# Kernel optimization log

Measured on AMD Instinct MI355X. Metric: run time of the kernel, lower is better.

The kernel has to match this reference:

```python
import jax, jax.numpy as jnp
import numpy as np

B, S, D, H = 2, 2048, 1024, 16
HD = D // H


def setup_inputs() -> dict:
    key = jax.random.key(0)
    ks = jax.random.split(key, 9)
    s = 1.0 / np.sqrt(D)
    return {
        "qx": jax.random.normal(ks[0], (B, S, D), jnp.float32),
        "kx": jax.random.normal(ks[1], (B, S, D), jnp.float32),
        "vx": jax.random.normal(ks[2], (B, S, D), jnp.float32),
        "mask": jnp.tril(jnp.ones((S, S), jnp.int32))[None, None],  # [1,1,S,S] causal
        "Wq": jax.random.uniform(ks[3], (D, D), jnp.float32, -s, s),
        "bq": jax.random.uniform(ks[4], (D,), jnp.float32, -s, s),
        "Wk": jax.random.uniform(ks[5], (D, D), jnp.float32, -s, s),
        "bk": jax.random.uniform(ks[6], (D,), jnp.float32, -s, s),
        "Wv": jax.random.uniform(ks[7], (D, D), jnp.float32, -s, s),
        "bv": jax.random.uniform(ks[8], (D,), jnp.float32, -s, s),
    }


def reference(qx, kx, vx, mask, Wq, bq, Wk, bk, Wv, bv):
    bat, seq_len, d_model = qx.shape
    # torch Linear: y = x @ W.T + b
    q = qx @ Wq.T + bq
    k = kx @ Wk.T + bk
    v = vx @ Wv.T + bv
    # [b, h, s, hd]
    q = q.reshape(bat, seq_len, H, HD).transpose(0, 2, 1, 3)
    k = k.reshape(bat, seq_len, H, HD).transpose(0, 2, 1, 3)
    v = v.reshape(bat, seq_len, H, HD).transpose(0, 2, 1, 3)
    # NOTE: original scales by sqrt(d_model), not sqrt(head_dim)
    attn_weight = jnp.einsum('bhqd,bhkd->bhqk', q, k) / jnp.sqrt(
        jnp.asarray(d_model, q.dtype))
    attn_weight = jnp.where(mask == 0, -jnp.inf, attn_weight)
    attn_score = jax.nn.softmax(attn_weight, axis=-1)
    attn_output = jnp.einsum('bhqk,bhkd->bhqd', attn_score, v)
    return attn_output.transpose(0, 2, 1, 3).reshape(bat, seq_len, d_model)
```

## Files before the change

kernel.cpp:

```cpp
#include <hip/hip_runtime.h>


typedef __attribute__((ext_vector_type(8))) short short8;
typedef __attribute__((ext_vector_type(4))) short shortx4;
typedef __attribute__((ext_vector_type(4))) float floatx4;

#define NEGBIG (-1.0e30f)
#define QSCALE 0.04508422002778011f

__device__ __forceinline__ float bf2f(ushort u) {
    union { unsigned int i; float f; } x; x.i = ((unsigned int)u) << 16; return x.f;
}
__device__ __forceinline__ ushort f2bf(float f) {
    union { unsigned int i; float f; } x; x.f = f;
    return (ushort)((x.i + 0x7FFFu + ((x.i >> 16) & 1u)) >> 16);
}
__device__ __forceinline__ void gl_lds16(const void* g, void* l) {
    __builtin_amdgcn_global_load_lds(
        (const __attribute__((address_space(1))) unsigned int*)g,
        (__attribute__((address_space(3))) unsigned int*)l, 16, 0, 0);
}

__global__ void detect_dtype(const unsigned int* __restrict__ w, int* __restrict__ flag) {
    const int lane = threadIdx.x;
    int hits = 0;
    for (int i = 0; i < 16; ++i) {
        unsigned int v = w[lane * 16 + i];
        int e = (int)((v >> 7) & 0xFF);
        hits += (e >= 100 && e <= 135) ? 1 : 0;
    }
    for (int off = 32; off; off >>= 1) hits += __shfl_down(hits, off);
    if (lane == 0) *flag = (hits > 512) ? 1 : 0;
}

__global__ void convert_fp32(
    const float* __restrict__ qx, const float* __restrict__ kx, const float* __restrict__ vx,
    const float* __restrict__ wq, const float* __restrict__ wk, const float* __restrict__ wv,
    const float* __restrict__ bq, const float* __restrict__ bk, const float* __restrict__ bv,
    ushort* __restrict__ dst, const int* __restrict__ flag)
{
    if (*flag) return;
    const int v = blockIdx.x * 256 + threadIdx.x;
    const float* src; int off = v;
    if      (v < 1048576) { src = qx; }
    else if (v < 2097152) { src = kx; off = v - 1048576; }
    else if (v < 3145728) { src = vx; off = v - 2097152; }
    else if (v < 3407872) { src = wq; off = v - 3145728; }
    else if (v < 3670016) { src = wk; off = v - 3407872; }
    else if (v < 3932160) { src = wv; off = v - 3670016; }
    else if (v < 3932416) { src = bq; off = v - 3932160; }
    else if (v < 3932672) { src = bk; off = v - 3932416; }
    else                  { src = bv; off = v - 3932672; }
    float4 f = ((const float4*)src)[off];
    shortx4 o;
    o[0] = (short)f2bf(f.x); o[1] = (short)f2bf(f.y);
    o[2] = (short)f2bf(f.z); o[3] = (short)f2bf(f.w);
    *(shortx4*)&dst[(size_t)v * 4] = o;
}

__global__ __launch_bounds__(256, 4) void qkv_gemm(
    const void* __restrict__ Xq_, const void* __restrict__ Wq_, const void* __restrict__ bq_,
    const void* __restrict__ Xk_, const void* __restrict__ Wk_, const void* __restrict__ bk_,
    const void* __restrict__ Xv_, const void* __restrict__ Wv_, const void* __restrict__ bv_,
    const ushort* __restrict__ conv,
    ushort* __restrict__ Yq, ushort* __restrict__ Yk, ushort* __restrict__ Yv,
    const int* __restrict__ flag)
{
    const int z  = blockIdx.z;
    const int dt = *flag;
    const ushort* X = dt ? (const ushort*)(z == 0 ? Xq_ : z == 1 ? Xk_ : Xv_)
                         : conv + (size_t)z * 4194304;
    const ushort* W = dt ? (const ushort*)(z == 0 ? Wq_ : z == 1 ? Wk_ : Wv_)
                         : conv + 12582912 + (size_t)z * 1048576;
    const ushort* bias = dt ? (const ushort*)(z == 0 ? bq_ : z == 1 ? bk_ : bv_)
                            : conv + 15728640 + z * 1024;
    ushort* Y = (z == 0) ? Yq : (z == 1) ? Yk : Yv;
    const float oscale = (z == 0) ? QSCALE : 1.0f;

    const int m0 = blockIdx.y * 128;
    const int n0 = blockIdx.x * 128;

    __shared__ __align__(16) ushort As[128 * 64];
    __shared__ __align__(16) ushort Bs[128 * 64];

    const int tid  = threadIdx.x;
    const int wave = tid >> 6;
    const int lane = tid & 63;
    const int col  = lane & 15;
    const int quad = lane >> 4;
    const int wm   = (wave >> 1) * 64;
    const int wn   = (wave & 1) * 64;

    floatx4 acc[4][4] = {};

    for (int k0 = 0; k0 < 1024; k0 += 64) {
        __syncthreads();
#pragma unroll
        for (int c = 0; c < 4; ++c) {
            const int o   = c * 4096 + tid * 16;
            const int row = o >> 7;
            const int bg  = ((o >> 4) & 7) ^ (row & 7);
            gl_lds16(X + (size_t)(m0 + row) * 1024 + k0 + bg * 8, &As[o >> 1]);
            gl_lds16(W + (size_t)(n0 + row) * 1024 + k0 + bg * 8, &Bs[o >> 1]);
        }
        __syncthreads();

#pragma unroll
        for (int h = 0; h < 2; ++h) {
            short8 af[4], bf_[4];
#pragma unroll
            for (int i = 0; i < 4; ++i) {
                const int ra = wm + i * 16 + col;
                const int rb = wn + i * 16 + col;
                af[i]  = *(const short8*)&As[ra * 64 + (((h * 4 + quad) ^ (ra & 7)) * 8)];
                bf_[i] = *(const short8*)&Bs[rb * 64 + (((h * 4 + quad) ^ (rb & 7)) * 8)];
            }
#pragma unroll
            for (int i = 0; i < 4; ++i)
#pragma unroll
                for (int j = 0; j < 4; ++j)
                    acc[i][j] = __builtin_amdgcn_mfma_f32_16x16x32_bf16(af[i], bf_[j], acc[i][j], 0, 0, 0);
        }
    }

    if (z == 2) {
#pragma unroll
        for (int j = 0; j < 4; ++j) {
            const int n = n0 + wn + j * 16 + col;
            const float bb = bf2f(bias[n]);
#pragma unroll
            for (int i = 0; i < 4; ++i) {
                const int m = m0 + wm + i * 16 + quad * 4;
                shortx4 pk;
#pragma unroll
                for (int r = 0; r < 4; ++r) pk[r] = (short)f2bf(acc[i][j][r] + bb);
                *(shortx4*)&Y[((size_t)(m >> 11) * 1024 + n) * 2048 + (m & 2047)] = pk;
            }
        }
    } else {
#pragma unroll
        for (int j = 0; j < 4; ++j) {
            const int n = n0 + wn + j * 16 + col;
            const float bb = bf2f(bias[n]);
#pragma unroll
            for (int i = 0; i < 4; ++i)
#pragma unroll
                for (int r = 0; r < 4; ++r) {
                    const int m = m0 + wm + i * 16 + quad * 4 + r;
                    Y[(size_t)m * 1024 + n] = f2bf((acc[i][j][r] + bb) * oscale);
                }
        }
    }
}

#define LDP 72

__global__ __launch_bounds__(256, 4) void attn(
    const ushort* __restrict__ Q, const ushort* __restrict__ K,
    const ushort* __restrict__ Vt, void* __restrict__ O,
    const int* __restrict__ flag)
{
    const int bx = blockIdx.x;
    const int h  = blockIdx.y;
    const int b  = blockIdx.z;
    const int dt = *flag;

    __shared__ __align__(16) ushort Qs[64 * 64];
    __shared__ __align__(16) ushort Ks[64 * 64];
    __shared__ __align__(16) ushort Vs[64 * 64];
    __shared__ __align__(16) ushort Ps[4][16 * LDP];

    const int tid  = threadIdx.x;
    const int wave = tid >> 6;
    const int lane = tid & 63;
    const int col  = lane & 15;
    const int quad = lane >> 4;

    const size_t qkbase = ((size_t)b * 2048) * 1024 + h * 64;
    const size_t vtbase = ((size_t)(b * 16 + h) * 64) * 2048;

    short8 ones;
#pragma unroll
    for (int i = 0; i < 8; ++i) ones[i] = (short)0x3F80;

    for (int seg = 0; seg < 2; ++seg) {
        const int qt = seg ? (31 - bx) : bx;
        const int q0 = qt * 64;

        __syncthreads();
#pragma unroll
        for (int c = 0; c < 2; ++c) {
            const int o   = c * 4096 + tid * 16;
            const int row = o >> 7;
            const int bg  = ((o >> 4) & 7) ^ (row & 7);
            gl_lds16(Q + qkbase + (size_t)(q0 + row) * 1024 + bg * 8, &Qs[o >> 1]);
        }
        __syncthreads();

        const int rq = wave * 16 + col;
        const short8 qf0 = *(const short8*)&Qs[rq * 64 + (((quad    ) ^ (col & 7)) * 8)];
        const short8 qf1 = *(const short8*)&Qs[rq * 64 + (((quad + 4) ^ (col & 7)) * 8)];

        floatx4 oacc[4] = {};
        floatx4 sacc = {};

        for (int t = 0; t <= qt; ++t) {
            const int kv0 = t * 64;
            __syncthreads();
#pragma unroll
            for (int c = 0; c < 2; ++c) {
                const int o   = c * 4096 + tid * 16;
                const int row = o >> 7;
                const int bg  = ((o >> 4) & 7) ^ (row & 7);
                gl_lds16(K  + qkbase + (size_t)(kv0 + row) * 1024 + bg * 8, &Ks[o >> 1]);
                gl_lds16(Vt + vtbase + (size_t)row * 2048 + kv0 + bg * 8,   &Vs[o >> 1]);
            }
            __syncthreads();

            floatx4 s4[4];
#pragma unroll
            for (int ct = 0; ct < 4; ++ct) {
                const int rk = ct * 16 + col;
                short8 kf0 = *(const short8*)&Ks[rk * 64 + (((quad    ) ^ (col & 7)) * 8)];
                short8 kf1 = *(const short8*)&Ks[rk * 64 + (((quad + 4) ^ (col & 7)) * 8)];
                floatx4 a = {};
                a = __builtin_amdgcn_mfma_f32_16x16x32_bf16(qf0, kf0, a, 0, 0, 0);
                a = __builtin_amdgcn_mfma_f32_16x16x32_bf16(qf1, kf1, a, 0, 0, 0);
                s4[ct] = a;
            }

            if (t == qt) {
#pragma unroll
                for (int ct = 0; ct < 4; ++ct) {
                    const int kidx = ct * 16 + col;
#pragma unroll
                    for (int r = 0; r < 4; ++r) {
                        const int qidx = wave * 16 + quad * 4 + r;
                        s4[ct][r] = (kidx <= qidx) ? s4[ct][r] : NEGBIG;
                    }
                }
            }

#pragma unroll
            for (int ct = 0; ct < 4; ++ct)
#pragma unroll
                for (int r = 0; r < 4; ++r) {
                    float p = __builtin_exp2f(s4[ct][r]);
                    Ps[wave][(quad * 4 + r) * LDP + ct * 16 + col] = f2bf(p);
                }

            short8 pf0 = *(const short8*)&Ps[wave][col * LDP + quad * 8];
            short8 pf1 = *(const short8*)&Ps[wave][col * LDP + 32 + quad * 8];

            sacc = __builtin_amdgcn_mfma_f32_16x16x32_bf16(pf0, ones, sacc, 0, 0, 0);
            sacc = __builtin_amdgcn_mfma_f32_16x16x32_bf16(pf1, ones, sacc, 0, 0, 0);

#pragma unroll
            for (int ct = 0; ct < 4; ++ct) {
                const int rv = ct * 16 + col;
                short8 vf0 = *(const short8*)&Vs[rv * 64 + (((quad    ) ^ (rv & 7)) * 8)];
                short8 vf1 = *(const short8*)&Vs[rv * 64 + (((quad + 4) ^ (rv & 7)) * 8)];
                oacc[ct] = __builtin_amdgcn_mfma_f32_16x16x32_bf16(pf0, vf0, oacc[ct], 0, 0, 0);
                oacc[ct] = __builtin_amdgcn_mfma_f32_16x16x32_bf16(pf1, vf1, oacc[ct], 0, 0, 0);
            }
        }

#pragma unroll
        for (int r = 0; r < 4; ++r) {
            const float inv = 1.0f / sacc[r];
            const int q = q0 + wave * 16 + quad * 4 + r;
#pragma unroll
            for (int ct = 0; ct < 4; ++ct) {
                const float v = oacc[ct][r] * inv;
                const size_t idx = ((size_t)b * 2048 + q) * 1024 + h * 64 + ct * 16 + col;
                if (dt) ((ushort*)O)[idx] = f2bf(v);
                else    ((float*)O)[idx]  = v;
            }
        }
    }
}

extern "C" void kernel_launch(void* const* d_in, const int* in_sizes, int n_in,
                              void* d_out, int out_size, void* d_ws, size_t ws_size,
                              hipStream_t stream) {
    const void* qx = d_in[0];
    const void* kx = d_in[1];
    const void* vx = d_in[2];
    const void* Wq = d_in[4]; const void* bq = d_in[5];
    const void* Wk = d_in[6]; const void* bk = d_in[7];
    const void* Wv = d_in[8]; const void* bv = d_in[9];

    int*    flag = (int*)d_ws;
    ushort* conv = (ushort*)((char*)d_ws + 256);
    ushort* Qw   = (ushort*)((char*)d_ws + 256 + 31463424);
    ushort* Kw   = Qw + (size_t)4096 * 1024;
    ushort* Vtw  = Kw + (size_t)4096 * 1024;

    detect_dtype<<<1, 64, 0, stream>>>((const unsigned int*)qx, flag);

    convert_fp32<<<15363, 256, 0, stream>>>(
        (const float*)qx, (const float*)kx, (const float*)vx,
        (const float*)Wq, (const float*)Wk, (const float*)Wv,
        (const float*)bq, (const float*)bk, (const float*)bv, conv, flag);

    dim3 gemm_grid(1024 / 128, 4096 / 128, 3);
    qkv_gemm<<<gemm_grid, 256, 0, stream>>>(qx, Wq, bq, kx, Wk, bk, vx, Wv, bv,
                                            conv, Qw, Kw, Vtw, flag);

    dim3 attn_grid(16, 16, 2);
    attn<<<attn_grid, 256, 0, stream>>>(Qw, Kw, Vtw, d_out, flag);
}
```

Baseline: 215.5 us.

## Double-buffer K/V tiles in attention to overlap loads with MFMA

Splits the K and V shared-memory tiles into two buffers and issues the async global-to-LDS loads for tile t+1 before computing on tile t. The first K/V tile is now loaded together with Q, and the loop keeps a single barrier at its end instead of two per iteration. This is meant to hide global load latency behind the QK and PV MFMAs, at the cost of more LDS per block, which may reduce occupancy. Whether async LDS loads have completed before the barrier depends on vmcnt waits that the compiler inserts.

```diff
diff --git a/kernel.cpp b/kernel.cpp
--- a/kernel.cpp
+++ b/kernel.cpp
@@ -166,8 +166,8 @@
     const int dt = *flag;
 
     __shared__ __align__(16) ushort Qs[64 * 64];
-    __shared__ __align__(16) ushort Ks[64 * 64];
-    __shared__ __align__(16) ushort Vs[64 * 64];
+    __shared__ __align__(16) ushort Ks[2][64 * 64];
+    __shared__ __align__(16) ushort Vs[2][64 * 64];
     __shared__ __align__(16) ushort Ps[4][16 * LDP];
 
     const int tid  = threadIdx.x;
@@ -183,18 +183,23 @@
 #pragma unroll
     for (int i = 0; i < 8; ++i) ones[i] = (short)0x3F80;
 
+    const int o0   = tid * 16;
+    const int o1   = 4096 + tid * 16;
+    const int row0 = o0 >> 7, row1 = o1 >> 7;
+    const int bg0  = ((o0 >> 4) & 7) ^ (row0 & 7);
+    const int bg1  = ((o1 >> 4) & 7) ^ (row1 & 7);
+
     for (int seg = 0; seg < 2; ++seg) {
         const int qt = seg ? (31 - bx) : bx;
         const int q0 = qt * 64;
 
         __syncthreads();
-#pragma unroll
-        for (int c = 0; c < 2; ++c) {
-            const int o   = c * 4096 + tid * 16;
-            const int row = o >> 7;
-            const int bg  = ((o >> 4) & 7) ^ (row & 7);
-            gl_lds16(Q + qkbase + (size_t)(q0 + row) * 1024 + bg * 8, &Qs[o >> 1]);
-        }
+        gl_lds16(Q + qkbase + (size_t)(q0 + row0) * 1024 + bg0 * 8, &Qs[o0 >> 1]);
+        gl_lds16(Q + qkbase + (size_t)(q0 + row1) * 1024 + bg1 * 8, &Qs[o1 >> 1]);
+        gl_lds16(K + qkbase + (size_t)row0 * 1024 + bg0 * 8, &Ks[0][o0 >> 1]);
+        gl_lds16(K + qkbase + (size_t)row1 * 1024 + bg1 * 8, &Ks[0][o1 >> 1]);
+        gl_lds16(Vt + vtbase + (size_t)row0 * 2048 + bg0 * 8, &Vs[0][o0 >> 1]);
+        gl_lds16(Vt + vtbase + (size_t)row1 * 2048 + bg1 * 8, &Vs[0][o1 >> 1]);
         __syncthreads();
 
         const int rq = wave * 16 + col;
@@ -205,24 +210,23 @@
         floatx4 sacc = {};
 
         for (int t = 0; t <= qt; ++t) {
-            const int kv0 = t * 64;
-            __syncthreads();
-#pragma unroll
-            for (int c = 0; c < 2; ++c) {
-                const int o   = c * 4096 + tid * 16;
-                const int row = o >> 7;
-                const int bg  = ((o >> 4) & 7) ^ (row & 7);
-                gl_lds16(K  + qkbase + (size_t)(kv0 + row) * 1024 + bg * 8, &Ks[o >> 1]);
-                gl_lds16(Vt + vtbase + (size_t)row * 2048 + kv0 + bg * 8,   &Vs[o >> 1]);
-            }
-            __syncthreads();
+            const int cur = t & 1;
+
+            if (t < qt) {
+                const int kv1 = (t + 1) * 64;
+                const int nb  = cur ^ 1;
+                gl_lds16(K + qkbase + (size_t)(kv1 + row0) * 1024 + bg0 * 8, &Ks[nb][o0 >> 1]);
+                gl_lds16(K + qkbase + (size_t)(kv1 + row1) * 1024 + bg1 * 8, &Ks[nb][o1 >> 1]);
+                gl_lds16(Vt + vtbase + (size_t)row0 * 2048 + kv1 + bg0 * 8, &Vs[nb][o0 >> 1]);
+                gl_lds16(Vt + vtbase + (size_t)row1 * 2048 + kv1 + bg1 * 8, &Vs[nb][o1 >> 1]);
+            }
 
             floatx4 s4[4];
 #pragma unroll
             for (int ct = 0; ct < 4; ++ct) {
                 const int rk = ct * 16 + col;
-                short8 kf0 = *(const short8*)&Ks[rk * 64 + (((quad    ) ^ (col & 7)) * 8)];
-                short8 kf1 = *(const short8*)&Ks[rk * 64 + (((quad + 4) ^ (col & 7)) * 8)];
+                short8 kf0 = *(const short8*)&Ks[cur][rk * 64 + (((quad    ) ^ (col & 7)) * 8)];
+                short8 kf1 = *(const short8*)&Ks[cur][rk * 64 + (((quad + 4) ^ (col & 7)) * 8)];
                 floatx4 a = {};
                 a = __builtin_amdgcn_mfma_f32_16x16x32_bf16(qf0, kf0, a, 0, 0, 0);
                 a = __builtin_amdgcn_mfma_f32_16x16x32_bf16(qf1, kf1, a, 0, 0, 0);
@@ -258,11 +262,13 @@
 #pragma unroll
             for (int ct = 0; ct < 4; ++ct) {
                 const int rv = ct * 16 + col;
-                short8 vf0 = *(const short8*)&Vs[rv * 64 + (((quad    ) ^ (rv & 7)) * 8)];
-                short8 vf1 = *(const short8*)&Vs[rv * 64 + (((quad + 4) ^ (rv & 7)) * 8)];
+                short8 vf0 = *(const short8*)&Vs[cur][rv * 64 + (((quad    ) ^ (rv & 7)) * 8)];
+                short8 vf1 = *(const short8*)&Vs[cur][rv * 64 + (((quad + 4) ^ (rv & 7)) * 8)];
                 oacc[ct] = __builtin_amdgcn_mfma_f32_16x16x32_bf16(pf0, vf0, oacc[ct], 0, 0, 0);
                 oacc[ct] = __builtin_amdgcn_mfma_f32_16x16x32_bf16(pf1, vf1, oacc[ct], 0, 0, 0);
             }
+
+            __syncthreads();
         }
 
 #pragma unroll
```

Result: faster. 209.6 us (-2.7%).
